# Kernel tuning notes

Measured on AMD Instinct MI355X. Metric: run time of the kernel, lower is better.

## Reference

```python
import jax, jax.numpy as jnp
import numpy as np

N = 50000
E = 800000
IN_DIM = 128
HID = 256


def _sage_conv(x, src, dst, W_l, b_l, W_r, num_nodes):
    # PyG SAGEConv (aggr='mean'): out = lin_l(mean_{j in N(i)} x_j) + lin_r(x_i)
    msgs = x[src]                                   # [E, D] gather of source feats
    agg = jax.ops.segment_sum(msgs, dst, num_segments=num_nodes)   # [N, D]
    deg = jax.ops.segment_sum(jnp.ones((src.shape[0],), dtype=x.dtype), dst,
                              num_segments=num_nodes)              # [N]
    agg = agg / jnp.maximum(deg, 1.0)[:, None]      # mean aggregation
    return agg @ W_l + b_l + x @ W_r


def setup_inputs() -> dict:
    key = jax.random.key(0)
    k = jax.random.split(key, 8)
    x = jax.random.normal(k[0], (N, IN_DIM), dtype=jnp.float32)
    edge_index = jax.random.randint(k[1], (2, E), 0, N, dtype=jnp.int64)
    s1 = 1.0 / np.sqrt(IN_DIM)
    s2 = 1.0 / np.sqrt(HID)
    W1_l = jax.random.uniform(k[2], (IN_DIM, HID), jnp.float32, -s1, s1)
    b1 = jax.random.uniform(k[3], (HID,), jnp.float32, -s1, s1)
    W1_r = jax.random.uniform(k[4], (IN_DIM, HID), jnp.float32, -s1, s1)
    W2_l = jax.random.uniform(k[5], (HID, HID), jnp.float32, -s2, s2)
    b2 = jax.random.uniform(k[6], (HID,), jnp.float32, -s2, s2)
    W2_r = jax.random.uniform(k[7], (HID, HID), jnp.float32, -s2, s2)
    return {"x": x, "edge_index": edge_index,
            "W1_l": W1_l, "b1": b1, "W1_r": W1_r,
            "W2_l": W2_l, "b2": b2, "W2_r": W2_r}


def reference(x, edge_index, W1_l, b1, W1_r, W2_l, b2, W2_r):
    src, dst = edge_index[0], edge_index[1]
    h = _sage_conv(x, src, dst, W1_l, b1, W1_r, N)   # [N, HID]
    h = jax.nn.relu(h)
    # dropout is identity in eval mode
    out = _sage_conv(h, src, dst, W2_l, b2, W2_r, N)  # [N, HID]
    return out
```

## Files before the change

kernel.cpp:

```cpp
#include <hip/hip_runtime.h>
#include <hip/hip_bf16.h>


typedef __attribute__((ext_vector_type(8))) short bf16x8;
typedef __attribute__((ext_vector_type(4))) float f32x4;
typedef __attribute__((ext_vector_type(4))) short s16x4;

constexpr int HIDC = 256;

__device__ __forceinline__ short f2bf(float v) {
  __hip_bfloat16 h = __float2bfloat16(v);
  return *reinterpret_cast<short*>(&h);
}
__device__ __forceinline__ float bf2f(short s) {
  unsigned int u = ((unsigned int)(unsigned short)s) << 16;
  float f;
  __builtin_memcpy(&f, &u, 4);
  return f;
}

__global__ __launch_bounds__(256) void deg_count_kernel(
    const int* __restrict__ dst, int* __restrict__ deg, int E, int N) {
  int e = blockIdx.x * blockDim.x + threadIdx.x;
  if (e < E) {
    int d = dst[e];
    if ((unsigned)d < (unsigned)N) atomicAdd(&deg[d], 1);
  }
}

__global__ __launch_bounds__(256) void blocksum_kernel(
    const int* __restrict__ deg, int* __restrict__ bsum, int N) {
  __shared__ int red[256];
  int i = blockIdx.x * 256 + threadIdx.x;
  red[threadIdx.x] = (i < N) ? deg[i] : 0;
  __syncthreads();
#pragma unroll
  for (int off = 128; off > 0; off >>= 1) {
    if (threadIdx.x < off) red[threadIdx.x] += red[threadIdx.x + off];
    __syncthreads();
  }
  if (threadIdx.x == 0) bsum[blockIdx.x] = red[0];
}

__global__ __launch_bounds__(256) void bscan_kernel(
    const int* __restrict__ bsum, int* __restrict__ boff,
    int* __restrict__ row_start, int nb, int N) {
  __shared__ int s[256];
  int t = threadIdx.x;
  s[t] = (t < nb) ? bsum[t] : 0;
  __syncthreads();
  for (int off = 1; off < 256; off <<= 1) {
    int v = (t >= off) ? s[t - off] : 0;
    __syncthreads();
    s[t] += v;
    __syncthreads();
  }
  if (t < nb) boff[t] = (t == 0) ? 0 : s[t - 1];
  if (t == nb - 1) row_start[N] = s[t];
}

__global__ __launch_bounds__(256) void scatter_offsets_kernel(
    const int* __restrict__ deg, const int* __restrict__ boff,
    int* __restrict__ row_start, int* __restrict__ cursor, int N) {
  __shared__ int s[256];
  int i = blockIdx.x * 256 + threadIdx.x;
  int t = threadIdx.x;
  int v = (i < N) ? deg[i] : 0;
  s[t] = v;
  __syncthreads();
  for (int off = 1; off < 256; off <<= 1) {
    int u = (t >= off) ? s[t - off] : 0;
    __syncthreads();
    s[t] += u;
    __syncthreads();
  }
  if (i < N) {
    int excl = s[t] - v + boff[blockIdx.x];
    row_start[i] = excl;
    cursor[i] = excl;
  }
}

__global__ __launch_bounds__(256) void fill_kernel(
    const int* __restrict__ src, const int* __restrict__ dst,
    int* __restrict__ cursor, int* __restrict__ esrc, int E, int N) {
  int e = blockIdx.x * blockDim.x + threadIdx.x;
  if (e < E) {
    int d = dst[e];
    if ((unsigned)d < (unsigned)N) {
      int p = atomicAdd(&cursor[d], 1);
      esrc[p] = src[e];
    }
  }
}

__global__ __launch_bounds__(256) void xconv_kernel(
    const float4* __restrict__ x, s16x4* __restrict__ hi,
    s16x4* __restrict__ lo, int total4) {
  int i = blockIdx.x * 256 + threadIdx.x;
  if (i >= total4) return;
  float4 v = x[i];
  s16x4 h, l;
  h.x = f2bf(v.x); l.x = f2bf(v.x - bf2f(h.x));
  h.y = f2bf(v.y); l.y = f2bf(v.y - bf2f(h.y));
  h.z = f2bf(v.z); l.z = f2bf(v.z - bf2f(h.z));
  h.w = f2bf(v.w); l.w = f2bf(v.w - bf2f(h.w));
  hi[i] = h;
  lo[i] = l;
}

template <int K, int NN>
__global__ __launch_bounds__(256) void wconv_kernel(
    const float* __restrict__ W, short* __restrict__ Wt_hi,
    short* __restrict__ Wt_lo) {
  int tid = blockIdx.x * 256 + threadIdx.x;
  if (tid >= K * NN) return;
  int k = tid / NN, n = tid % NN;
  float v = W[tid];
  short hv = f2bf(v);
  Wt_hi[n * K + k] = hv;
  Wt_lo[n * K + k] = f2bf(v - bf2f(hv));
}

__global__ __launch_bounds__(256) void gather1_kernel(
    const short* __restrict__ xhi, const int* __restrict__ row_start,
    const int* __restrict__ esrc, short* __restrict__ ahi,
    short* __restrict__ alo, int N) {
  int gid = (int)(((long long)blockIdx.x * 256 + threadIdx.x) >> 4);
  int l = threadIdx.x & 15;
  if (gid >= N) return;
  int lo_e = row_start[gid], hi_e = row_start[gid + 1];
  float acc[8];
#pragma unroll
  for (int j = 0; j < 8; ++j) acc[j] = 0.f;
  int e = lo_e;
  for (; e + 3 < hi_e; e += 4) {
    bf16x8 v0 = *(const bf16x8*)(xhi + (size_t)esrc[e] * 128 + l * 8);
    bf16x8 v1 = *(const bf16x8*)(xhi + (size_t)esrc[e + 1] * 128 + l * 8);
    bf16x8 v2 = *(const bf16x8*)(xhi + (size_t)esrc[e + 2] * 128 + l * 8);
    bf16x8 v3 = *(const bf16x8*)(xhi + (size_t)esrc[e + 3] * 128 + l * 8);
#pragma unroll
    for (int j = 0; j < 8; ++j)
      acc[j] += (bf2f(v0[j]) + bf2f(v1[j])) + (bf2f(v2[j]) + bf2f(v3[j]));
  }
  for (; e < hi_e; ++e) {
    bf16x8 v0 = *(const bf16x8*)(xhi + (size_t)esrc[e] * 128 + l * 8);
#pragma unroll
    for (int j = 0; j < 8; ++j) acc[j] += bf2f(v0[j]);
  }
  float inv = (hi_e > lo_e) ? 1.0f / (float)(hi_e - lo_e) : 0.0f;
  bf16x8 oh, ol;
#pragma unroll
  for (int j = 0; j < 8; ++j) {
    float v = acc[j] * inv;
    short hv = f2bf(v);
    oh[j] = hv;
    ol[j] = f2bf(v - bf2f(hv));
  }
  *(bf16x8*)(ahi + (size_t)gid * 128 + l * 8) = oh;
  *(bf16x8*)(alo + (size_t)gid * 128 + l * 8) = ol;
}

__global__ __launch_bounds__(256) void gather2_kernel(
    const short* __restrict__ hhi, const int* __restrict__ row_start,
    const int* __restrict__ esrc, short* __restrict__ ahi,
    short* __restrict__ alo, int N) {
  int gid = (int)(((long long)blockIdx.x * 256 + threadIdx.x) >> 5);
  int l = threadIdx.x & 31;
  if (gid >= N) return;
  int lo_e = row_start[gid], hi_e = row_start[gid + 1];
  float acc[8];
#pragma unroll
  for (int j = 0; j < 8; ++j) acc[j] = 0.f;
  int e = lo_e;
  for (; e + 3 < hi_e; e += 4) {
    bf16x8 v0 = *(const bf16x8*)(hhi + (size_t)esrc[e] * HIDC + l * 8);
    bf16x8 v1 = *(const bf16x8*)(hhi + (size_t)esrc[e + 1] * HIDC + l * 8);
    bf16x8 v2 = *(const bf16x8*)(hhi + (size_t)esrc[e + 2] * HIDC + l * 8);
    bf16x8 v3 = *(const bf16x8*)(hhi + (size_t)esrc[e + 3] * HIDC + l * 8);
#pragma unroll
    for (int j = 0; j < 8; ++j)
      acc[j] += (bf2f(v0[j]) + bf2f(v1[j])) + (bf2f(v2[j]) + bf2f(v3[j]));
  }
  for (; e < hi_e; ++e) {
    bf16x8 v0 = *(const bf16x8*)(hhi + (size_t)esrc[e] * HIDC + l * 8);
#pragma unroll
    for (int j = 0; j < 8; ++j) acc[j] += bf2f(v0[j]);
  }
  float inv = (hi_e > lo_e) ? 1.0f / (float)(hi_e - lo_e) : 0.0f;
  bf16x8 oh, ol;
#pragma unroll
  for (int j = 0; j < 8; ++j) {
    float v = acc[j] * inv;
    short hv = f2bf(v);
    oh[j] = hv;
    ol[j] = f2bf(v - bf2f(hv));
  }
  *(bf16x8*)(ahi + (size_t)gid * HIDC + l * 8) = oh;
  *(bf16x8*)(alo + (size_t)gid * HIDC + l * 8) = ol;
}

template <int K1, bool RELU, bool OUTBF>
__global__ __launch_bounds__(256) void mfma_gemm(
    const short* __restrict__ Ahi, const short* __restrict__ Alo,
    const short* __restrict__ Xhi, const short* __restrict__ Xlo,
    const short* __restrict__ WLhi, const short* __restrict__ WLlo,
    const short* __restrict__ WRhi, const short* __restrict__ WRlo,
    const float* __restrict__ bias, float* __restrict__ Cf,
    short* __restrict__ Chi, short* __restrict__ Clo, int M) {
  __shared__ __align__(16) short As_hi[128][40];
  __shared__ __align__(16) short As_lo[128][40];
  __shared__ __align__(16) short Bs_hi[128][40];
  __shared__ __align__(16) short Bs_lo[128][40];

  const int tid = threadIdx.x;
  const int lane = tid & 63;
  const int w = tid >> 6;
  const int brow = blockIdx.y * 128;
  const int bcol = blockIdx.x * 128;
  const int wr = (w >> 1) * 64;
  const int wc = (w & 1) * 64;

  const int srow = tid >> 1;
  const int koff = (tid & 1) * 16;

  int arow = brow + srow;
  if (arow >= M) arow = M - 1;
  const int bn = bcol + srow;

  f32x4 acc[4][4];
#pragma unroll
  for (int m = 0; m < 4; ++m)
#pragma unroll
    for (int n = 0; n < 4; ++n) acc[m][n] = (f32x4){0.f, 0.f, 0.f, 0.f};

  for (int k0 = 0; k0 < 2 * K1; k0 += 32) {
    const bool left = k0 < K1;
    const int kk = left ? k0 : k0 - K1;
    const short* __restrict__ Aph = left ? Ahi : Xhi;
    const short* __restrict__ Apl = left ? Alo : Xlo;
    const short* __restrict__ Bph = left ? WLhi : WRhi;
    const short* __restrict__ Bpl = left ? WLlo : WRlo;

    size_t abase = (size_t)arow * K1 + kk + koff;
    size_t bbase = (size_t)bn * K1 + kk + koff;
    bf16x8 ga0 = *(const bf16x8*)(Aph + abase);
    bf16x8 ga1 = *(const bf16x8*)(Aph + abase + 8);
    bf16x8 ga2 = *(const bf16x8*)(Apl + abase);
    bf16x8 ga3 = *(const bf16x8*)(Apl + abase + 8);
    bf16x8 gb0 = *(const bf16x8*)(Bph + bbase);
    bf16x8 gb1 = *(const bf16x8*)(Bph + bbase + 8);
    bf16x8 gb2 = *(const bf16x8*)(Bpl + bbase);
    bf16x8 gb3 = *(const bf16x8*)(Bpl + bbase + 8);

    __syncthreads();
    *(bf16x8*)&As_hi[srow][koff] = ga0;
    *(bf16x8*)&As_hi[srow][koff + 8] = ga1;
    *(bf16x8*)&As_lo[srow][koff] = ga2;
    *(bf16x8*)&As_lo[srow][koff + 8] = ga3;
    *(bf16x8*)&Bs_hi[srow][koff] = gb0;
    *(bf16x8*)&Bs_hi[srow][koff + 8] = gb1;
    *(bf16x8*)&Bs_lo[srow][koff] = gb2;
    *(bf16x8*)&Bs_lo[srow][koff + 8] = gb3;
    __syncthreads();

    const int fr = lane & 15;
    const int fk = (lane >> 4) * 8;
    bf16x8 ah[4], al[4], bh[4], bl[4];
#pragma unroll
    for (int m = 0; m < 4; ++m) {
      ah[m] = *(const bf16x8*)&As_hi[wr + m * 16 + fr][fk];
      al[m] = *(const bf16x8*)&As_lo[wr + m * 16 + fr][fk];
    }
#pragma unroll
    for (int n = 0; n < 4; ++n) {
      bh[n] = *(const bf16x8*)&Bs_hi[wc + n * 16 + fr][fk];
      bl[n] = *(const bf16x8*)&Bs_lo[wc + n * 16 + fr][fk];
    }
#pragma unroll
    for (int m = 0; m < 4; ++m)
#pragma unroll
      for (int n = 0; n < 4; ++n) {
        acc[m][n] = __builtin_amdgcn_mfma_f32_16x16x32_bf16(ah[m], bh[n],
                                                            acc[m][n], 0, 0, 0);
        acc[m][n] = __builtin_amdgcn_mfma_f32_16x16x32_bf16(ah[m], bl[n],
                                                            acc[m][n], 0, 0, 0);
        acc[m][n] = __builtin_amdgcn_mfma_f32_16x16x32_bf16(al[m], bh[n],
                                                            acc[m][n], 0, 0, 0);
      }
  }

  const int lcol = lane & 15;
  const int lrow = (lane >> 4) * 4;
#pragma unroll
  for (int m = 0; m < 4; ++m) {
    int gr0 = brow + wr + m * 16 + lrow;
#pragma unroll
    for (int n = 0; n < 4; ++n) {
      int gc = bcol + wc + n * 16 + lcol;
      float bv = bias[gc];
#pragma unroll
      for (int j = 0; j < 4; ++j) {
        int gr = gr0 + j;
        if (gr >= M) continue;
        float v = acc[m][n][j] + bv;
        if (RELU) v = fmaxf(v, 0.f);
        if (OUTBF) {
          short hv = f2bf(v);
          Chi[(size_t)gr * HIDC + gc] = hv;
          Clo[(size_t)gr * HIDC + gc] = f2bf(v - bf2f(hv));
        } else {
          Cf[(size_t)gr * HIDC + gc] = v;
        }
      }
    }
  }
}

extern "C" void kernel_launch(void* const* d_in, const int* in_sizes, int n_in,
                              void* d_out, int out_size, void* d_ws,
                              size_t ws_size, hipStream_t stream) {
  const float* x = (const float*)d_in[0];
  const int* ei = (const int*)d_in[1];
  const float* W1l = (const float*)d_in[2];
  const float* b1 = (const float*)d_in[3];
  const float* W1r = (const float*)d_in[4];
  const float* W2l = (const float*)d_in[5];
  const float* b2 = (const float*)d_in[6];
  const float* W2r = (const float*)d_in[7];
  float* out = (float*)d_out;

  const int N = in_sizes[0] / 128;
  const int E = in_sizes[1] / 2;
  const int* src = ei;
  const int* dst = ei + E;

  char* ws = (char*)d_ws;
  size_t off = 0;
  auto walloc = [&](size_t bytes) {
    void* p = ws + off;
    off += (bytes + 255) & ~(size_t)255;
    return p;
  };
  int* deg = (int*)walloc((size_t)N * 4);
  int* row_start = (int*)walloc((size_t)(N + 1) * 4);
  int* cursor = (int*)walloc((size_t)N * 4);
  int* esrc = (int*)walloc((size_t)E * 4);
  int* bsum = (int*)walloc(256 * 4);
  int* boff = (int*)walloc(256 * 4);
  short* x_hi = (short*)walloc((size_t)N * 128 * 2);
  short* x_lo = (short*)walloc((size_t)N * 128 * 2);
  short* agg1_hi = (short*)walloc((size_t)N * 128 * 2);
  short* agg1_lo = (short*)walloc((size_t)N * 128 * 2);
  short* h_hi = (short*)walloc((size_t)N * 256 * 2);
  short* h_lo = (short*)walloc((size_t)N * 256 * 2);
  short* agg2_hi = (short*)walloc((size_t)N * 256 * 2);
  short* agg2_lo = (short*)walloc((size_t)N * 256 * 2);
  short* Wt1l_hi = (short*)walloc(128 * 256 * 2);
  short* Wt1l_lo = (short*)walloc(128 * 256 * 2);
  short* Wt1r_hi = (short*)walloc(128 * 256 * 2);
  short* Wt1r_lo = (short*)walloc(128 * 256 * 2);
  short* Wt2l_hi = (short*)walloc(256 * 256 * 2);
  short* Wt2l_lo = (short*)walloc(256 * 256 * 2);
  short* Wt2r_hi = (short*)walloc(256 * 256 * 2);
  short* Wt2r_lo = (short*)walloc(256 * 256 * 2);
  (void)ws_size;
  (void)n_in;
  (void)out_size;

  const int BLK = 256;
  const int eblocks = (E + BLK - 1) / BLK;
  const int nblocks = (N + BLK - 1) / BLK;

  xconv_kernel<<<(N * 32 + BLK - 1) / BLK, BLK, 0, stream>>>(
      (const float4*)x, (s16x4*)x_hi, (s16x4*)x_lo, N * 32);
  wconv_kernel<128, 256><<<(128 * 256 + BLK - 1) / BLK, BLK, 0, stream>>>(
      W1l, Wt1l_hi, Wt1l_lo);
  wconv_kernel<128, 256><<<(128 * 256 + BLK - 1) / BLK, BLK, 0, stream>>>(
      W1r, Wt1r_hi, Wt1r_lo);
  wconv_kernel<256, 256><<<(256 * 256 + BLK - 1) / BLK, BLK, 0, stream>>>(
      W2l, Wt2l_hi, Wt2l_lo);
  wconv_kernel<256, 256><<<(256 * 256 + BLK - 1) / BLK, BLK, 0, stream>>>(
      W2r, Wt2r_hi, Wt2r_lo);

  hipMemsetAsync(deg, 0, (size_t)N * 4, stream);
  deg_count_kernel<<<eblocks, BLK, 0, stream>>>(dst, deg, E, N);
  blocksum_kernel<<<nblocks, BLK, 0, stream>>>(deg, bsum, N);
  bscan_kernel<<<1, 256, 0, stream>>>(bsum, boff, row_start, nblocks, N);
  scatter_offsets_kernel<<<nblocks, BLK, 0, stream>>>(deg, boff, row_start,
                                                      cursor, N);
  fill_kernel<<<eblocks, BLK, 0, stream>>>(src, dst, cursor, esrc, E, N);

  gather1_kernel<<<(N * 16 + BLK - 1) / BLK, BLK, 0, stream>>>(
      x_hi, row_start, esrc, agg1_hi, agg1_lo, N);
  {
    dim3 grid(2, (N + 127) / 128);
    mfma_gemm<128, true, true><<<grid, BLK, 0, stream>>>(
        agg1_hi, agg1_lo, x_hi, x_lo, Wt1l_hi, Wt1l_lo, Wt1r_hi, Wt1r_lo, b1,
        nullptr, h_hi, h_lo, N);
  }

  gather2_kernel<<<(N * 32 + BLK - 1) / BLK, BLK, 0, stream>>>(
      h_hi, row_start, esrc, agg2_hi, agg2_lo, N);
  {
    dim3 grid(2, (N + 127) / 128);
    mfma_gemm<256, false, false><<<grid, BLK, 0, stream>>>(
        agg2_hi, agg2_lo, h_hi, h_lo, Wt2l_hi, Wt2l_lo, Wt2r_hi, Wt2r_lo, b2,
        out, nullptr, nullptr, N);
  }
}
```

Measured before the change: 420.1 us.

## Widen GEMM tile to full 256 columns with XOR-swizzled LDS layout

The GEMM block now covers 128 rows by all 256 output columns. Each wave owns a 64-column slice across all 128 rows, so the A tile is loaded once per row block instead of twice and the grid is halved. The LDS writes and reads use an XOR swizzle on alternate rows to reduce bank conflicts, and launch bounds request two blocks per CU. The cost is a doubled accumulator array (128 floats per thread), which adds register pressure, plus more LDS and global loads per block.

```diff
diff --git a/kernel.cpp b/kernel.cpp
--- a/kernel.cpp
+++ b/kernel.cpp
@@ -200,8 +200,10 @@
   *(bf16x8*)(alo + (size_t)gid * HIDC + l * 8) = ol;
 }
 
+#define SWZ(row, c) ((c) ^ (((row) & 1) << 4))
+
 template <int K1, bool RELU, bool OUTBF>
-__global__ __launch_bounds__(256) void mfma_gemm(
+__global__ __launch_bounds__(256, 2) void mfma_gemm(
     const short* __restrict__ Ahi, const short* __restrict__ Alo,
     const short* __restrict__ Xhi, const short* __restrict__ Xlo,
     const short* __restrict__ WLhi, const short* __restrict__ WLlo,
@@ -210,27 +212,25 @@
     short* __restrict__ Chi, short* __restrict__ Clo, int M) {
   __shared__ __align__(16) short As_hi[128][40];
   __shared__ __align__(16) short As_lo[128][40];
-  __shared__ __align__(16) short Bs_hi[128][40];
-  __shared__ __align__(16) short Bs_lo[128][40];
+  __shared__ __align__(16) short Bs_hi[256][40];
+  __shared__ __align__(16) short Bs_lo[256][40];
 
   const int tid = threadIdx.x;
   const int lane = tid & 63;
   const int w = tid >> 6;
-  const int brow = blockIdx.y * 128;
-  const int bcol = blockIdx.x * 128;
-  const int wr = (w >> 1) * 64;
-  const int wc = (w & 1) * 64;
+  const int brow = blockIdx.x * 128;
+  const int wc = w * 64;
 
   const int srow = tid >> 1;
   const int koff = (tid & 1) * 16;
+  const int skoff = SWZ(srow, koff);
 
   int arow = brow + srow;
   if (arow >= M) arow = M - 1;
-  const int bn = bcol + srow;
-
-  f32x4 acc[4][4];
-#pragma unroll
-  for (int m = 0; m < 4; ++m)
+
+  f32x4 acc[8][4];
+#pragma unroll
+  for (int m = 0; m < 8; ++m)
 #pragma unroll
     for (int n = 0; n < 4; ++n) acc[m][n] = (f32x4){0.f, 0.f, 0.f, 0.f};
 
@@ -243,61 +243,72 @@
     const short* __restrict__ Bpl = left ? WLlo : WRlo;
 
     size_t abase = (size_t)arow * K1 + kk + koff;
-    size_t bbase = (size_t)bn * K1 + kk + koff;
-    bf16x8 ga0 = *(const bf16x8*)(Aph + abase);
-    bf16x8 ga1 = *(const bf16x8*)(Aph + abase + 8);
-    bf16x8 ga2 = *(const bf16x8*)(Apl + abase);
-    bf16x8 ga3 = *(const bf16x8*)(Apl + abase + 8);
-    bf16x8 gb0 = *(const bf16x8*)(Bph + bbase);
-    bf16x8 gb1 = *(const bf16x8*)(Bph + bbase + 8);
-    bf16x8 gb2 = *(const bf16x8*)(Bpl + bbase);
-    bf16x8 gb3 = *(const bf16x8*)(Bpl + bbase + 8);
-
-    __syncthreads();
-    *(bf16x8*)&As_hi[srow][koff] = ga0;
-    *(bf16x8*)&As_hi[srow][koff + 8] = ga1;
-    *(bf16x8*)&As_lo[srow][koff] = ga2;
-    *(bf16x8*)&As_lo[srow][koff + 8] = ga3;
-    *(bf16x8*)&Bs_hi[srow][koff] = gb0;
-    *(bf16x8*)&Bs_hi[srow][koff + 8] = gb1;
-    *(bf16x8*)&Bs_lo[srow][koff] = gb2;
-    *(bf16x8*)&Bs_lo[srow][koff + 8] = gb3;
+    size_t bbase0 = (size_t)srow * K1 + kk + koff;
+    size_t bbase1 = (size_t)(srow + 128) * K1 + kk + koff;
+    bf16x8 gah0 = *(const bf16x8*)(Aph + abase);
+    bf16x8 gah1 = *(const bf16x8*)(Aph + abase + 8);
+    bf16x8 gal0 = *(const bf16x8*)(Apl + abase);
+    bf16x8 gal1 = *(const bf16x8*)(Apl + abase + 8);
+    bf16x8 gbh00 = *(const bf16x8*)(Bph + bbase0);
+    bf16x8 gbh01 = *(const bf16x8*)(Bph + bbase0 + 8);
+    bf16x8 gbh10 = *(const bf16x8*)(Bph + bbase1);
+    bf16x8 gbh11 = *(const bf16x8*)(Bph + bbase1 + 8);
+    bf16x8 gbl00 = *(const bf16x8*)(Bpl + bbase0);
+    bf16x8 gbl01 = *(const bf16x8*)(Bpl + bbase0 + 8);
+    bf16x8 gbl10 = *(const bf16x8*)(Bpl + bbase1);
+    bf16x8 gbl11 = *(const bf16x8*)(Bpl + bbase1 + 8);
+
+    __syncthreads();
+    *(bf16x8*)&As_hi[srow][skoff] = gah0;
+    *(bf16x8*)&As_hi[srow][skoff + 8] = gah1;
+    *(bf16x8*)&As_lo[srow][skoff] = gal0;
+    *(bf16x8*)&As_lo[srow][skoff + 8] = gal1;
+    *(bf16x8*)&Bs_hi[srow][skoff] = gbh00;
+    *(bf16x8*)&Bs_hi[srow][skoff + 8] = gbh01;
+    *(bf16x8*)&Bs_hi[srow + 128][skoff] = gbh10;
+    *(bf16x8*)&Bs_hi[srow + 128][skoff + 8] = gbh11;
+    *(bf16x8*)&Bs_lo[srow][skoff] = gbl00;
+    *(bf16x8*)&Bs_lo[srow][skoff + 8] = gbl01;
+    *(bf16x8*)&Bs_lo[srow + 128][skoff] = gbl10;
+    *(bf16x8*)&Bs_lo[srow + 128][skoff + 8] = gbl11;
     __syncthreads();
 
     const int fr = lane & 15;
     const int fk = (lane >> 4) * 8;
-    bf16x8 ah[4], al[4], bh[4], bl[4];
-#pragma unroll
-    for (int m = 0; m < 4; ++m) {
-      ah[m] = *(const bf16x8*)&As_hi[wr + m * 16 + fr][fk];
-      al[m] = *(const bf16x8*)&As_lo[wr + m * 16 + fr][fk];
+    bf16x8 bh[4], bl[4];
+#pragma unroll
+    for (int n = 0; n < 4; ++n) {
+      int br = wc + n * 16 + fr;
+      int fks = SWZ(br, fk);
+      bh[n] = *(const bf16x8*)&Bs_hi[br][fks];
+      bl[n] = *(const bf16x8*)&Bs_lo[br][fks];
     }
 #pragma unroll
-    for (int n = 0; n < 4; ++n) {
-      bh[n] = *(const bf16x8*)&Bs_hi[wc + n * 16 + fr][fk];
-      bl[n] = *(const bf16x8*)&Bs_lo[wc + n * 16 + fr][fk];
-    }
-#pragma unroll
-    for (int m = 0; m < 4; ++m)
+    for (int m = 0; m < 8; ++m) {
+      int ar = m * 16 + fr;
+      int fks = SWZ(ar, fk);
+      bf16x8 ah = *(const bf16x8*)&As_hi[ar][fks];
+      bf16x8 al = *(const bf16x8*)&As_lo[ar][fks];
 #pragma unroll
       for (int n = 0; n < 4; ++n) {
-        acc[m][n] = __builtin_amdgcn_mfma_f32_16x16x32_bf16(ah[m], bh[n],
+        acc[m][n] = __builtin_amdgcn_mfma_f32_16x16x32_bf16(ah, bh[n],
                                                             acc[m][n], 0, 0, 0);
-        acc[m][n] = __builtin_amdgcn_mfma_f32_16x16x32_bf16(ah[m], bl[n],
+        acc[m][n] = __builtin_amdgcn_mfma_f32_16x16x32_bf16(ah, bl[n],
                                                             acc[m][n], 0, 0, 0);
-        acc[m][n] = __builtin_amdgcn_mfma_f32_16x16x32_bf16(al[m], bh[n],
+        acc[m][n] = __builtin_amdgcn_mfma_f32_16x16x32_bf16(al, bh[n],
                                                             acc[m][n], 0, 0, 0);
       }
+    }
   }
 
   const int lcol = lane & 15;
   const int lrow = (lane >> 4) * 4;
 #pragma unroll
-  for (int m = 0; m < 4; ++m) {
-    int gr0 = brow + wr + m * 16 + lrow;
+  for (int m = 0; m < 8; ++m) {
+    int gr0 = brow + m * 16 + lrow;
 #pragma unroll
     for (int n = 0; n < 4; ++n) {
-      int gc = bcol + wc + n * 16 + lcol;
+      int gc = wc + n * 16 + lcol;
       float bv = bias[gc];
 #pragma unroll
       for (int j = 0; j < 4; ++j) {
@@ -394,7 +405,7 @@
   gather1_kernel<<<(N * 16 + BLK - 1) / BLK, BLK, 0, stream>>>(
       x_hi, row_start, esrc, agg1_hi, agg1_lo, N);
   {
-    dim3 grid(2, (N + 127) / 128);
+    dim3 grid((N + 127) / 128);
     mfma_gemm<128, true, true><<<grid, BLK, 0, stream>>>(
         agg1_hi, agg1_lo, x_hi, x_lo, Wt1l_hi, Wt1l_lo, Wt1r_hi, Wt1r_lo, b1,
         nullptr, h_hi, h_lo, N);
@@ -403,7 +414,7 @@
   gather2_kernel<<<(N * 32 + BLK - 1) / BLK, BLK, 0, stream>>>(
       h_hi, row_start, esrc, agg2_hi, agg2_lo, N);
   {
-    dim3 grid(2, (N + 127) / 128);
+    dim3 grid((N + 127) / 128);
     mfma_gemm<256, false, false><<<grid, BLK, 0, stream>>>(
         agg2_hi, agg2_lo, h_hi, h_lo, Wt2l_hi, Wt2l_lo, Wt2r_hi, Wt2r_lo, b2,
         out, nullptr, nullptr, N);
```

New measurement: 407.3 us. 1.03x faster.

## Use direct global-to-LDS loads with XOR swizzle in GEMM; atomic-free CSR fill

Applied to the files above, without the earlier changes.

The GEMM tile loads now use global_load_lds to write straight into shared memory. The padded LDS rows become unpadded 32-wide rows with an XOR swizzle to avoid bank conflicts. The launch grid is transposed so consecutive blocks share the same weight column tile, launch bounds request 4 waves per SIMD, and A fragments are loaded per m-iteration to reduce register pressure. The CSR build now records each edge's rank during degree counting, so the fill pass needs no second atomic. This costs an extra E-sized rank array.

```diff
diff --git a/kernel.cpp b/kernel.cpp
--- a/kernel.cpp
+++ b/kernel.cpp
@@ -19,12 +19,19 @@
   return f;
 }
 
-__global__ __launch_bounds__(256) void deg_count_kernel(
-    const int* __restrict__ dst, int* __restrict__ deg, int E, int N) {
+__device__ __forceinline__ void gll16(const short* g, short* l) {
+  __builtin_amdgcn_global_load_lds(
+      (const __attribute__((address_space(1))) unsigned int*)g,
+      (__attribute__((address_space(3))) unsigned int*)l, 16, 0, 0);
+}
+
+__global__ __launch_bounds__(256) void deg_rank_kernel(
+    const int* __restrict__ dst, int* __restrict__ deg, int* __restrict__ rank,
+    int E, int N) {
   int e = blockIdx.x * blockDim.x + threadIdx.x;
   if (e < E) {
     int d = dst[e];
-    if ((unsigned)d < (unsigned)N) atomicAdd(&deg[d], 1);
+    if ((unsigned)d < (unsigned)N) rank[e] = atomicAdd(&deg[d], 1);
   }
 }
 
@@ -61,7 +68,7 @@
 
 __global__ __launch_bounds__(256) void scatter_offsets_kernel(
     const int* __restrict__ deg, const int* __restrict__ boff,
-    int* __restrict__ row_start, int* __restrict__ cursor, int N) {
+    int* __restrict__ row_start, int N) {
   __shared__ int s[256];
   int i = blockIdx.x * 256 + threadIdx.x;
   int t = threadIdx.x;
@@ -74,23 +81,17 @@
     s[t] += u;
     __syncthreads();
   }
-  if (i < N) {
-    int excl = s[t] - v + boff[blockIdx.x];
-    row_start[i] = excl;
-    cursor[i] = excl;
-  }
-}
-
-__global__ __launch_bounds__(256) void fill_kernel(
+  if (i < N) row_start[i] = s[t] - v + boff[blockIdx.x];
+}
+
+__global__ __launch_bounds__(256) void fill2_kernel(
     const int* __restrict__ src, const int* __restrict__ dst,
-    int* __restrict__ cursor, int* __restrict__ esrc, int E, int N) {
+    const int* __restrict__ rank, const int* __restrict__ row_start,
+    int* __restrict__ esrc, int E, int N) {
   int e = blockIdx.x * blockDim.x + threadIdx.x;
   if (e < E) {
     int d = dst[e];
-    if ((unsigned)d < (unsigned)N) {
-      int p = atomicAdd(&cursor[d], 1);
-      esrc[p] = src[e];
-    }
+    if ((unsigned)d < (unsigned)N) esrc[row_start[d] + rank[e]] = src[e];
   }
 }
 
@@ -201,38 +202,55 @@
 }
 
 template <int K1, bool RELU, bool OUTBF>
-__global__ __launch_bounds__(256) void mfma_gemm(
+__global__ __launch_bounds__(256, 4) void mfma_gemm(
     const short* __restrict__ Ahi, const short* __restrict__ Alo,
     const short* __restrict__ Xhi, const short* __restrict__ Xlo,
     const short* __restrict__ WLhi, const short* __restrict__ WLlo,
     const short* __restrict__ WRhi, const short* __restrict__ WRlo,
     const float* __restrict__ bias, float* __restrict__ Cf,
     short* __restrict__ Chi, short* __restrict__ Clo, int M) {
-  __shared__ __align__(16) short As_hi[128][40];
-  __shared__ __align__(16) short As_lo[128][40];
-  __shared__ __align__(16) short Bs_hi[128][40];
-  __shared__ __align__(16) short Bs_lo[128][40];
+  __shared__ __align__(16) short As_hi[128][32];
+  __shared__ __align__(16) short As_lo[128][32];
+  __shared__ __align__(16) short Bs_hi[128][32];
+  __shared__ __align__(16) short Bs_lo[128][32];
 
   const int tid = threadIdx.x;
   const int lane = tid & 63;
   const int w = tid >> 6;
-  const int brow = blockIdx.y * 128;
-  const int bcol = blockIdx.x * 128;
-  const int wr = (w >> 1) * 64;
-  const int wc = (w & 1) * 64;
-
-  const int srow = tid >> 1;
-  const int koff = (tid & 1) * 16;
-
-  int arow = brow + srow;
-  if (arow >= M) arow = M - 1;
-  const int bn = bcol + srow;
+  const int brow = blockIdx.x * 128;
+  const int bcol = blockIdx.y * 128;
+  const int wrl = (w >> 1) * 64;
+  const int wcl = (w & 1) * 64;
+
+  const int lrow = lane >> 2;
+  const int lc = lane & 3;
+  const int r1 = 16 * w + lrow;
+  const int r2 = 64 + 16 * w + lrow;
+  const int ga1 = min(brow + r1, M - 1);
+  const int ga2 = min(brow + r2, M - 1);
+  const int sw1 = (lc ^ ((r1 >> 1) & 3)) << 3;
+  const int sw2 = (lc ^ ((r2 >> 1) & 3)) << 3;
+  const size_t aoff1 = (size_t)ga1 * K1 + sw1;
+  const size_t aoff2 = (size_t)ga2 * K1 + sw2;
+  const size_t boff1 = (size_t)(bcol + r1) * K1 + sw1;
+  const size_t boff2 = (size_t)(bcol + r2) * K1 + sw2;
+  short* const lAh1 = &As_hi[16 * w][0];
+  short* const lAh2 = &As_hi[64 + 16 * w][0];
+  short* const lAl1 = &As_lo[16 * w][0];
+  short* const lAl2 = &As_lo[64 + 16 * w][0];
+  short* const lBh1 = &Bs_hi[16 * w][0];
+  short* const lBh2 = &Bs_hi[64 + 16 * w][0];
+  short* const lBl1 = &Bs_lo[16 * w][0];
+  short* const lBl2 = &Bs_lo[64 + 16 * w][0];
 
   f32x4 acc[4][4];
 #pragma unroll
   for (int m = 0; m < 4; ++m)
 #pragma unroll
     for (int n = 0; n < 4; ++n) acc[m][n] = (f32x4){0.f, 0.f, 0.f, 0.f};
+
+  const int fr = lane & 15;
+  const int q = lane >> 4;
 
   for (int k0 = 0; k0 < 2 * K1; k0 += 32) {
     const bool left = k0 < K1;
@@ -242,62 +260,51 @@
     const short* __restrict__ Bph = left ? WLhi : WRhi;
     const short* __restrict__ Bpl = left ? WLlo : WRlo;
 
-    size_t abase = (size_t)arow * K1 + kk + koff;
-    size_t bbase = (size_t)bn * K1 + kk + koff;
-    bf16x8 ga0 = *(const bf16x8*)(Aph + abase);
-    bf16x8 ga1 = *(const bf16x8*)(Aph + abase + 8);
-    bf16x8 ga2 = *(const bf16x8*)(Apl + abase);
-    bf16x8 ga3 = *(const bf16x8*)(Apl + abase + 8);
-    bf16x8 gb0 = *(const bf16x8*)(Bph + bbase);
-    bf16x8 gb1 = *(const bf16x8*)(Bph + bbase + 8);
-    bf16x8 gb2 = *(const bf16x8*)(Bpl + bbase);
-    bf16x8 gb3 = *(const bf16x8*)(Bpl + bbase + 8);
-
-    __syncthreads();
-    *(bf16x8*)&As_hi[srow][koff] = ga0;
-    *(bf16x8*)&As_hi[srow][koff + 8] = ga1;
-    *(bf16x8*)&As_lo[srow][koff] = ga2;
-    *(bf16x8*)&As_lo[srow][koff + 8] = ga3;
-    *(bf16x8*)&Bs_hi[srow][koff] = gb0;
-    *(bf16x8*)&Bs_hi[srow][koff + 8] = gb1;
-    *(bf16x8*)&Bs_lo[srow][koff] = gb2;
-    *(bf16x8*)&Bs_lo[srow][koff + 8] = gb3;
-    __syncthreads();
-
-    const int fr = lane & 15;
-    const int fk = (lane >> 4) * 8;
-    bf16x8 ah[4], al[4], bh[4], bl[4];
+    __syncthreads();
+    gll16(Aph + aoff1 + kk, lAh1);
+    gll16(Aph + aoff2 + kk, lAh2);
+    gll16(Apl + aoff1 + kk, lAl1);
+    gll16(Apl + aoff2 + kk, lAl2);
+    gll16(Bph + boff1 + kk, lBh1);
+    gll16(Bph + boff2 + kk, lBh2);
+    gll16(Bpl + boff1 + kk, lBl1);
+    gll16(Bpl + boff2 + kk, lBl2);
+    __syncthreads();
+
+    bf16x8 bh[4], bl[4];
+#pragma unroll
+    for (int n = 0; n < 4; ++n) {
+      int r = wcl + n * 16 + fr;
+      int off = r * 32 + ((q ^ ((r >> 1) & 3)) << 3);
+      bh[n] = *(const bf16x8*)(&Bs_hi[0][0] + off);
+      bl[n] = *(const bf16x8*)(&Bs_lo[0][0] + off);
+    }
 #pragma unroll
     for (int m = 0; m < 4; ++m) {
-      ah[m] = *(const bf16x8*)&As_hi[wr + m * 16 + fr][fk];
-      al[m] = *(const bf16x8*)&As_lo[wr + m * 16 + fr][fk];
-    }
-#pragma unroll
-    for (int n = 0; n < 4; ++n) {
-      bh[n] = *(const bf16x8*)&Bs_hi[wc + n * 16 + fr][fk];
-      bl[n] = *(const bf16x8*)&Bs_lo[wc + n * 16 + fr][fk];
-    }
-#pragma unroll
-    for (int m = 0; m < 4; ++m)
+      int r = wrl + m * 16 + fr;
+      int off = r * 32 + ((q ^ ((r >> 1) & 3)) << 3);
+      bf16x8 ah = *(const bf16x8*)(&As_hi[0][0] + off);
+      bf16x8 al = *(const bf16x8*)(&As_lo[0][0] + off);
 #pragma unroll
       for (int n = 0; n < 4; ++n) {
-        acc[m][n] = __builtin_amdgcn_mfma_f32_16x16x32_bf16(ah[m], bh[n],
+        acc[m][n] = __builtin_amdgcn_mfma_f32_16x16x32_bf16(ah, bh[n],
                                                             acc[m][n], 0, 0, 0);
-        acc[m][n] = __builtin_amdgcn_mfma_f32_16x16x32_bf16(ah[m], bl[n],
+        acc[m][n] = __builtin_amdgcn_mfma_f32_16x16x32_bf16(ah, bl[n],
                                                             acc[m][n], 0, 0, 0);
-        acc[m][n] = __builtin_amdgcn_mfma_f32_16x16x32_bf16(al[m], bh[n],
+        acc[m][n] = __builtin_amdgcn_mfma_f32_16x16x32_bf16(al, bh[n],
                                                             acc[m][n], 0, 0, 0);
       }
+    }
   }
 
   const int lcol = lane & 15;
-  const int lrow = (lane >> 4) * 4;
+  const int lrw = (lane >> 4) * 4;
 #pragma unroll
   for (int m = 0; m < 4; ++m) {
-    int gr0 = brow + wr + m * 16 + lrow;
+    int gr0 = brow + wrl + m * 16 + lrw;
 #pragma unroll
     for (int n = 0; n < 4; ++n) {
-      int gc = bcol + wc + n * 16 + lcol;
+      int gc = bcol + wcl + n * 16 + lcol;
       float bv = bias[gc];
 #pragma unroll
       for (int j = 0; j < 4; ++j) {
@@ -344,7 +351,7 @@
   };
   int* deg = (int*)walloc((size_t)N * 4);
   int* row_start = (int*)walloc((size_t)(N + 1) * 4);
-  int* cursor = (int*)walloc((size_t)N * 4);
+  int* rank = (int*)walloc((size_t)E * 4);
   int* esrc = (int*)walloc((size_t)E * 4);
   int* bsum = (int*)walloc(256 * 4);
   int* boff = (int*)walloc(256 * 4);
@@ -384,17 +391,17 @@
       W2r, Wt2r_hi, Wt2r_lo);
 
   hipMemsetAsync(deg, 0, (size_t)N * 4, stream);
-  deg_count_kernel<<<eblocks, BLK, 0, stream>>>(dst, deg, E, N);
+  deg_rank_kernel<<<eblocks, BLK, 0, stream>>>(dst, deg, rank, E, N);
   blocksum_kernel<<<nblocks, BLK, 0, stream>>>(deg, bsum, N);
   bscan_kernel<<<1, 256, 0, stream>>>(bsum, boff, row_start, nblocks, N);
-  scatter_offsets_kernel<<<nblocks, BLK, 0, stream>>>(deg, boff, row_start,
-                                                      cursor, N);
-  fill_kernel<<<eblocks, BLK, 0, stream>>>(src, dst, cursor, esrc, E, N);
+  scatter_offsets_kernel<<<nblocks, BLK, 0, stream>>>(deg, boff, row_start, N);
+  fill2_kernel<<<eblocks, BLK, 0, stream>>>(src, dst, rank, row_start, esrc, E,
+                                            N);
 
   gather1_kernel<<<(N * 16 + BLK - 1) / BLK, BLK, 0, stream>>>(
       x_hi, row_start, esrc, agg1_hi, agg1_lo, N);
   {
-    dim3 grid(2, (N + 127) / 128);
+    dim3 grid((N + 127) / 128, 2);
     mfma_gemm<128, true, true><<<grid, BLK, 0, stream>>>(
         agg1_hi, agg1_lo, x_hi, x_lo, Wt1l_hi, Wt1l_lo, Wt1r_hi, Wt1r_lo, b1,
         nullptr, h_hi, h_lo, N);
@@ -403,7 +410,7 @@
   gather2_kernel<<<(N * 32 + BLK - 1) / BLK, BLK, 0, stream>>>(
       h_hi, row_start, esrc, agg2_hi, agg2_lo, N);
   {
-    dim3 grid(2, (N + 127) / 128);
+    dim3 grid((N + 127) / 128, 2);
     mfma_gemm<256, false, false><<<grid, BLK, 0, stream>>>(
         agg2_hi, agg2_lo, h_hi, h_lo, Wt2l_hi, Wt2l_lo, Wt2r_hi, Wt2r_lo, b2,
         out, nullptr, nullptr, N);
```

New measurement: 361.8 us. -13.9%, faster.
